# Kernel optimization log

Measured on AMD Instinct MI355X. Metric: run time of the kernel, lower is better.

The kernel has to match this reference:

```python
import jax, jax.numpy as jnp
import numpy as np
import math

D_MODEL = 1024
NUM_HEADS = 16
HEAD_DIM = D_MODEL // NUM_HEADS
BATCH = 2
SEQ = 2048
NEG_INF = -1000000.0  # matches torch code's -1e6 fill


def setup_inputs() -> dict:
    key = jax.random.key(0)
    ks = jax.random.split(key, 10)
    s = 1.0 / math.sqrt(D_MODEL)
    inp = {
        "X": jax.random.normal(ks[0], (BATCH, SEQ, D_MODEL), dtype=jnp.float32),
        "Wq": jax.random.uniform(ks[1], (D_MODEL, D_MODEL), minval=-s, maxval=s, dtype=jnp.float32),
        "bq": jnp.zeros((D_MODEL,), jnp.float32),
        "Wk": jax.random.uniform(ks[2], (D_MODEL, D_MODEL), minval=-s, maxval=s, dtype=jnp.float32),
        "bk": jnp.zeros((D_MODEL,), jnp.float32),
        "Wv": jax.random.uniform(ks[3], (D_MODEL, D_MODEL), minval=-s, maxval=s, dtype=jnp.float32),
        "bv": jnp.zeros((D_MODEL,), jnp.float32),
        "Wo": jax.random.uniform(ks[4], (D_MODEL, D_MODEL), minval=-s, maxval=s, dtype=jnp.float32),
        "bo": jnp.zeros((D_MODEL,), jnp.float32),
        "valid_lens": jax.random.randint(ks[5], (BATCH, NUM_HEADS), 1, SEQ + 1, dtype=jnp.int64)
        if jax.config.jax_enable_x64 else
        jax.random.randint(ks[5], (BATCH, NUM_HEADS), 1, SEQ + 1, dtype=jnp.int32),
    }
    return inp


def _split_heads(Y, B, S):
    # (B, S, D) -> (B*H, S, head_dim), matching transpose_qkv
    return Y.reshape(B, S, NUM_HEADS, HEAD_DIM).transpose(0, 2, 1, 3).reshape(B * NUM_HEADS, S, HEAD_DIM)


def reference(X, Wq, bq, Wk, bk, Wv, bv, Wo, bo, valid_lens):
    B, S, D = X.shape
    q = _split_heads(X @ Wq.T + bq, B, S)
    k = _split_heads(X @ Wk.T + bk, B, S)
    v = _split_heads(X @ Wv.T + bv, B, S)
    scores = jnp.einsum("bqd,bkd->bqk", q, k) / math.sqrt(HEAD_DIM)  # (B*H, S, S)
    # Faithful to torch code: 2-D valid_lens reshaped to (B*H,), mask over
    # the first two dims -> entire query rows j >= valid_len set to -1e6.
    row_mask = jnp.arange(S)[None, :] < valid_lens.reshape(-1)[:, None]  # (B*H, S)
    scores = jnp.where(row_mask[:, :, None], scores, NEG_INF)
    attn = jax.nn.softmax(scores, axis=-1)
    out = jnp.einsum("bqk,bkd->bqd", attn, v)  # (B*H, S, head_dim)
    out = out.reshape(B, NUM_HEADS, S, HEAD_DIM).transpose(0, 2, 1, 3).reshape(B, S, D)
    return out @ Wo.T + bo
```

## Files before the change

### kernel.cpp

```cpp
#include <hip/hip_runtime.h>

#define SQ 2048
#define DM 1024
#define NH 16
#define HD 64

typedef __bf16 bf16x8 __attribute__((ext_vector_type(8)));
typedef float f32x4 __attribute__((ext_vector_type(4)));
typedef unsigned short u16;
typedef unsigned int u32;

__device__ __forceinline__ u16 f2b(float f) {
  union { float f; u32 u; } c; c.f = f;
  return (u16)((c.u + 0x7FFFu + ((c.u >> 16) & 1u)) >> 16);
}

__device__ __forceinline__ void gll16(const void* g, void* l) {
  __builtin_amdgcn_global_load_lds(
      (const __attribute__((address_space(1))) void*)g,
      (__attribute__((address_space(3))) void*)l, 16, 0, 0);
}

__global__ void __launch_bounds__(256) conv_bf16(
    const float* __restrict__ X,
    const float* __restrict__ Wq, const float* __restrict__ Wk,
    const float* __restrict__ Wv, const float* __restrict__ Wo,
    u16* __restrict__ Xb, u16* __restrict__ Wqb, u16* __restrict__ Wkb,
    u16* __restrict__ Wvb, u16* __restrict__ Wob) {
  const size_t e = ((size_t)blockIdx.x * 256 + threadIdx.x) * 8;
  const float* src; u16* dst; size_t rel;
  if (e < 4194304u)      { src = X;  dst = Xb;  rel = e; }
  else if (e < 5242880u) { src = Wq; dst = Wqb; rel = e - 4194304u; }
  else if (e < 6291456u) { src = Wk; dst = Wkb; rel = e - 5242880u; }
  else if (e < 7340032u) { src = Wv; dst = Wvb; rel = e - 6291456u; }
  else                   { src = Wo; dst = Wob; rel = e - 7340032u; }
  float4 a = *(const float4*)(src + rel);
  float4 b = *(const float4*)(src + rel + 4);
  union { u16 h[8]; uint4 v; } o;
  o.h[0] = f2b(a.x); o.h[1] = f2b(a.y); o.h[2] = f2b(a.z); o.h[3] = f2b(a.w);
  o.h[4] = f2b(b.x); o.h[5] = f2b(b.y); o.h[6] = f2b(b.z); o.h[7] = f2b(b.w);
  *(uint4*)(dst + rel) = o.v;
}

__global__ void __launch_bounds__(256) mean_v2(
    const u16* __restrict__ Vt, const int* __restrict__ vlen,
    u16* __restrict__ Ao, int* __restrict__ wl) {
  __shared__ float part[256];
  __shared__ float smv[64];
  const int bh = blockIdx.x, c8 = blockIdx.y;
  const int t = threadIdx.x, d = t >> 2, c = t & 3;
  const u16* row = Vt + ((size_t)bh * HD + d) * SQ + c * 512;
  float s = 0.f;
  for (int i = 0; i < 64; ++i) {
    bf16x8 v = *(const bf16x8*)(row + i * 8);
    s += ((float)v[0] + (float)v[1]) + ((float)v[2] + (float)v[3])
       + ((float)v[4] + (float)v[5]) + ((float)v[6] + (float)v[7]);
  }
  part[t] = s;
  __syncthreads();
  if (c == 0) {
    const float tot = (part[t] + part[t + 1]) + (part[t + 2] + part[t + 3]);
    smv[d] = tot * (1.0f / 2048.0f);
  }
  __syncthreads();

  const int vl = vlen[bh];
  const int ft = (vl + 63) >> 6;
  const int b = bh >> 4, h = bh & 15;
  const int c16 = t & 15, r16 = t >> 4;
  union { u16 h4[4]; uint2 u; } pv;
#pragma unroll
  for (int j = 0; j < 4; ++j) pv.h4[j] = f2b(smv[c16 * 4 + j]);
  for (int ss = ft * 64 + c8 * 16 + r16; ss < SQ; ss += 128)
    *(uint2*)(Ao + ((size_t)(b * SQ + ss)) * DM + h * HD + c16 * 4) = pv.u;

  if (bh == 0 && c8 == 0) {
    __shared__ int nts[32], off[32];
    if (t < 32) {
      int nt = (vlen[t] + 63) >> 6;
      if (nt > 32) nt = 32;
      nts[t] = nt;
    }
    __syncthreads();
    if (t == 0) {
      int acc = 0;
      for (int i = 0; i < 32; ++i) { off[i] = acc; acc += nts[i]; }
      wl[0] = acc;
    }
    __syncthreads();
    if (t < 32) {
      const int o = off[t], nt = nts[t];
      for (int q = 0; q < nt; ++q) wl[1 + o + q] = (t << 5) | q;
    }
  }
}

__global__ void __launch_bounds__(256, 3) qkv_gemm(
    const u16* __restrict__ Xb, const u16* __restrict__ Wqkv,
    const float* __restrict__ bq, const float* __restrict__ bk, const float* __restrict__ bv,
    const int* __restrict__ vlen,
    u16* __restrict__ Qb, u16* __restrict__ Kb, u16* __restrict__ Vt) {
  __shared__ u16 sA[3][4096];
  __shared__ u16 sB[3][4096];
  const int id = blockIdx.x;
  const int swz = (id & 7) * 96 + (id >> 3);
  const int bx = swz % 24, by = swz / 24;
  const int m0 = by * 128, n0 = bx * 128;
  const int mode = n0 >> 10;
  const float* bias = (mode == 0) ? bq : (mode == 1) ? bk : bv;

  if (mode == 0) {
    const int bb = m0 >> 11, s0 = m0 & 2047, h0 = n0 >> 6;
    if (s0 >= vlen[bb * NH + h0] && s0 >= vlen[bb * NH + h0 + 1]) return;
  }

  const int t = threadIdx.x, l = t & 63, w = t >> 6;
  const int wr = w >> 1, wc = w & 1, lg = l >> 4, li = l & 15;

  int srcOff[2];
#pragma unroll
  for (int j = 0; j < 2; ++j) {
    const int g = w * 2 + j;
    const int row = g * 16 + (l >> 2);
    const int colsrc = ((l & 3) * 8) ^ (((row >> 3) & 1) << 4);
    srcOff[j] = row * DM + colsrc;
  }
  const u16* Abase = Xb + (size_t)m0 * DM;
  const u16* Bbase = Wqkv + (size_t)n0 * DM;

  auto stage = [&](int buf, int kt) {
#pragma unroll
    for (int j = 0; j < 2; ++j) {
      gll16(Abase + srcOff[j] + kt * 32, &sA[buf][(w * 2 + j) * 512]);
      gll16(Bbase + srcOff[j] + kt * 32, &sB[buf][(w * 2 + j) * 512]);
    }
  };

  f32x4 acc[4][4];
  f32x4 z4 = {0.f, 0.f, 0.f, 0.f};
#pragma unroll
  for (int i = 0; i < 4; ++i)
#pragma unroll
    for (int j = 0; j < 4; ++j) acc[i][j] = z4;

  stage(0, 0);
  stage(1, 1);
  for (int kt = 0; kt < 32; ++kt) {
    const int bsel = kt % 3;
    if (kt < 31) asm volatile("s_waitcnt vmcnt(4)" ::: "memory");
    else         asm volatile("s_waitcnt vmcnt(0)" ::: "memory");
    __builtin_amdgcn_s_barrier();
    asm volatile("" ::: "memory");

    bf16x8 aF[4], bF[4];
#pragma unroll
    for (int mi = 0; mi < 4; ++mi) {
      const int rl = wr * 64 + mi * 16 + li;
      aF[mi] = *(const bf16x8*)(&sA[bsel][rl * 32 + ((lg * 8) ^ (((rl >> 3) & 1) << 4))]);
    }
#pragma unroll
    for (int ni = 0; ni < 4; ++ni) {
      const int rn = wc * 64 + ni * 16 + li;
      bF[ni] = *(const bf16x8*)(&sB[bsel][rn * 32 + ((lg * 8) ^ (((rn >> 3) & 1) << 4))]);
    }
    if (kt + 2 < 32) stage((kt + 2) % 3, kt + 2);

    __builtin_amdgcn_s_setprio(1);
#pragma unroll
    for (int mi = 0; mi < 4; ++mi)
#pragma unroll
      for (int ni = 0; ni < 4; ++ni)
        acc[mi][ni] = __builtin_amdgcn_mfma_f32_16x16x32_bf16(aF[mi], bF[ni], acc[mi][ni], 0, 0, 0);
    __builtin_amdgcn_s_setprio(0);
  }

#pragma unroll
  for (int mi = 0; mi < 4; ++mi) {
    const int m = m0 + wr * 64 + mi * 16 + lg * 4;
    const int b = m >> 11;
    const int s = m & 2047;
#pragma unroll
    for (int ni = 0; ni < 4; ++ni) {
      const int n = n0 + wc * 64 + ni * 16 + li;
      const int nn = n - (mode << 10);
      const int h = nn >> 6, dd = nn & 63;
      const float bia = bias[nn];
      const size_t bh = (size_t)(b * NH + h);
      if (mode == 2) {
        union { u16 h4[4]; uint2 u; } pk;
#pragma unroll
        for (int r = 0; r < 4; ++r) pk.h4[r] = f2b(acc[mi][ni][r] + bia);
        *(uint2*)(Vt + (bh * HD + dd) * SQ + s) = pk.u;
      } else {
#pragma unroll
        for (int r = 0; r < 4; ++r) {
          const float val = acc[mi][ni][r] + bia;
          const int ss = s + r;
          if (mode == 0) Qb[(bh * SQ + ss) * HD + dd] = f2b(val * 0.180336880f);
          else           Kb[(bh * SQ + ss) * HD + dd] = f2b(val);
        }
      }
    }
  }
}

__global__ void __launch_bounds__(256) out_gemm(
    const u16* __restrict__ Ag, const u16* __restrict__ Wob,
    const float* __restrict__ bo, float* __restrict__ out) {
  __shared__ u16 sA[2][2048];
  __shared__ u16 sB[2][4096];
  const int t = threadIdx.x, l = t & 63, w = t >> 6;
  const int wr = w >> 1, wc = w & 1, lg = l >> 4, li = l & 15;
  const int m0 = blockIdx.y * 64, n0 = blockIdx.x * 128;

  auto stage = [&](int buf, int kt) {
    {
      const int s = w * 64 + l;
      const int r = s >> 2, cc = s & 3;
      gll16(Ag + (size_t)(m0 + r) * DM + kt * 32 + cc * 8, &sA[buf][w * 512]);
    }
#pragma unroll
    for (int c = 0; c < 2; ++c) {
      const int g = w * 2 + c;
      const int s = g * 64 + l;
      const int r = s >> 2, cc = s & 3;
      gll16(Wob + (size_t)(n0 + r) * DM + kt * 32 + cc * 8, &sB[buf][g * 512]);
    }
  };

  f32x4 acc[2][4];
  f32x4 z4 = {0.f, 0.f, 0.f, 0.f};
#pragma unroll
  for (int i = 0; i < 2; ++i)
#pragma unroll
    for (int j = 0; j < 4; ++j) acc[i][j] = z4;

  stage(0, 0);
  __syncthreads();
  int cur = 0;
  for (int kt = 0; kt < DM / 32; ++kt) {
    if (kt + 1 < DM / 32) stage(cur ^ 1, kt + 1);
    bf16x8 aF[2], bF[4];
#pragma unroll
    for (int mi = 0; mi < 2; ++mi)
      aF[mi] = *(const bf16x8*)(&sA[cur][(wr * 32 + mi * 16 + li) * 32 + lg * 8]);
#pragma unroll
    for (int ni = 0; ni < 4; ++ni)
      bF[ni] = *(const bf16x8*)(&sB[cur][(wc * 64 + ni * 16 + li) * 32 + lg * 8]);
#pragma unroll
    for (int mi = 0; mi < 2; ++mi)
#pragma unroll
      for (int ni = 0; ni < 4; ++ni)
        acc[mi][ni] = __builtin_amdgcn_mfma_f32_16x16x32_bf16(aF[mi], bF[ni], acc[mi][ni], 0, 0, 0);
    __syncthreads();
    cur ^= 1;
  }

#pragma unroll
  for (int mi = 0; mi < 2; ++mi) {
    const int m = m0 + wr * 32 + mi * 16 + lg * 4;
#pragma unroll
    for (int ni = 0; ni < 4; ++ni) {
      const int n = n0 + wc * 64 + ni * 16 + li;
      const float bia = bo[n];
#pragma unroll
      for (int r = 0; r < 4; ++r)
        out[(size_t)(m + r) * DM + n] = acc[mi][ni][r] + bia;
    }
  }
}

__global__ void __launch_bounds__(256, 2) attn_v15(
    const u16* __restrict__ Qb, const u16* __restrict__ Kb, const u16* __restrict__ Vt,
    const int* __restrict__ vlen, const int* __restrict__ wl, u16* __restrict__ Ao) {
  __shared__ u16 sKV[4][10240];
  const int t = threadIdx.x, w = t >> 6, l = t & 63, lg = l >> 4, li = l & 15;
  const int nit = wl[0];

  int kOff[4], vOff[4];
#pragma unroll
  for (int i = 0; i < 4; ++i) {
    {
      const int s = i * 64 + l, row = s >> 3, c = s & 7;
      const int csrc = c ^ (row & 7);
      const int sig = (((row >> 2) & 3) << 3) | (((row >> 4) & 1) << 2) | (row & 3);
      kOff[i] = sig * HD + csrc * 8;
    }
    {
      const int s = i * 64 + l, d = s >> 2, c = s & 3;
      const int csrc = c ^ ((d >> 2) & 3);
      vOff[i] = d * SQ + csrc * 8;
    }
  }

  u16* sw = &sKV[w][0];
  f32x4* op = (f32x4*)&sKV[0][0];
  float* lp = (float*)((char*)&sKV[0][0] + 65536);

  for (int it = blockIdx.x; it < nit; it += gridDim.x) {
    const int item = wl[1 + it];
    const int bh = item >> 5, qt = item & 31;
    const int vl = vlen[bh];
    const int q0 = qt * 64;
    const int b = bh >> 4, h = bh & 15;
    const u16* Qh = Qb + (size_t)bh * SQ * HD;
    const u16* Kh = Kb + (size_t)bh * SQ * HD;
    const u16* Vh = Vt + (size_t)bh * HD * SQ;
    const int k0 = w * 512;

    bf16x8 qf[4][2];
#pragma unroll
    for (int g = 0; g < 4; ++g) {
      const bool mq = (q0 + g * 16 + li) >= vl;
#pragma unroll
      for (int kk = 0; kk < 2; ++kk) {
        qf[g][kk] = *(const bf16x8*)(Qh + (size_t)(q0 + g * 16 + li) * HD + kk * 32 + lg * 8);
        if (mq) {
          union { u32 u[4]; bf16x8 v; } z; z.u[0] = z.u[1] = z.u[2] = z.u[3] = 0;
          qf[g][kk] = z.v;
        }
      }
    }

    auto stageK = [&](int buf, int tt) {
      const u16* kb = Kh + (size_t)(k0 + tt * 32) * HD;
#pragma unroll
      for (int i = 0; i < 4; ++i) gll16(kb + kOff[i], sw + buf * 2048 + i * 512);
    };
    auto stageV = [&](int buf, int tt) {
      const u16* vb = Vh + (size_t)(k0 + tt * 32);
#pragma unroll
      for (int i = 0; i < 4; ++i) gll16(vb + vOff[i], sw + 6144 + buf * 2048 + i * 512);
    };

    f32x4 z4 = {0.f, 0.f, 0.f, 0.f};
    f32x4 acc[4][4];
    float lr[4] = {0.f, 0.f, 0.f, 0.f};
#pragma unroll
    for (int g = 0; g < 4; ++g)
#pragma unroll
      for (int n2 = 0; n2 < 4; ++n2) acc[g][n2] = z4;

    stageV(0, 0); stageK(0, 0); stageK(1, 1);
    for (int tt = 0; tt < 16; ++tt) {
      if (tt + 1 < 16) stageV((tt + 1) & 1, tt + 1);
      if (tt + 2 < 16) stageK((tt + 2) % 3, tt + 2);
      if (tt <= 13)      asm volatile("s_waitcnt vmcnt(12)" ::: "memory");
      else if (tt == 14) asm volatile("s_waitcnt vmcnt(8)" ::: "memory");
      else               asm volatile("s_waitcnt vmcnt(0)" ::: "memory");
      const u16* kb_ = sw + (tt % 3) * 2048;
      const u16* vb_ = sw + 6144 + (tt & 1) * 2048;

      bf16x8 kf[2][2], vf[4];
#pragma unroll
      for (int ni = 0; ni < 2; ++ni) {
        const int row = ni * 16 + li;
        kf[ni][0] = *(const bf16x8*)(kb_ + row * 64 + ((lg ^ (row & 7)) * 8));
        kf[ni][1] = *(const bf16x8*)(kb_ + row * 64 + (((4 + lg) ^ (row & 7)) * 8));
      }
#pragma unroll
      for (int n2 = 0; n2 < 4; ++n2) {
        const int d = n2 * 16 + li;
        vf[n2] = *(const bf16x8*)(vb_ + d * 32 + ((lg ^ ((d >> 2) & 3)) * 8));
      }

      f32x4 s0a[4], s1a[4];
      __builtin_amdgcn_s_setprio(1);
#pragma unroll
      for (int g = 0; g < 4; ++g) {
        s0a[g] = __builtin_amdgcn_mfma_f32_16x16x32_bf16(kf[0][0], qf[g][0], z4, 0, 0, 0);
        s1a[g] = __builtin_amdgcn_mfma_f32_16x16x32_bf16(kf[1][0], qf[g][0], z4, 0, 0, 0);
      }
#pragma unroll
      for (int g = 0; g < 4; ++g) {
        s0a[g] = __builtin_amdgcn_mfma_f32_16x16x32_bf16(kf[0][1], qf[g][1], s0a[g], 0, 0, 0);
        s1a[g] = __builtin_amdgcn_mfma_f32_16x16x32_bf16(kf[1][1], qf[g][1], s1a[g], 0, 0, 0);
      }
      __builtin_amdgcn_s_setprio(0);

      bf16x8 Pv[4];
#pragma unroll
      for (int g = 0; g < 4; ++g) {
        union { __bf16 e[8]; bf16x8 v; } P;
        float ls = 0.f;
#pragma unroll
        for (int r = 0; r < 4; ++r) {
          const float p0 = __builtin_amdgcn_exp2f(s0a[g][r]);
          const float p1 = __builtin_amdgcn_exp2f(s1a[g][r]);
          P.e[r]     = (__bf16)p0;
          P.e[4 + r] = (__bf16)p1;
          ls += p0 + p1;
        }
        lr[g] += ls;
        Pv[g] = P.v;
      }

      __builtin_amdgcn_s_setprio(1);
#pragma unroll
      for (int g = 0; g < 4; ++g)
#pragma unroll
        for (int n2 = 0; n2 < 4; ++n2)
          acc[g][n2] = __builtin_amdgcn_mfma_f32_16x16x32_bf16(vf[n2], Pv[g], acc[g][n2], 0, 0, 0);
      __builtin_amdgcn_s_setprio(0);
    }

    __syncthreads();
#pragma unroll
    for (int g = 0; g < 4; ++g) {
#pragma unroll
      for (int n2 = 0; n2 < 4; ++n2)
        op[(((w * 4) + g) * 4 + n2) * 64 + l] = acc[g][n2];
      float v = lr[g];
      v += __shfl_xor(v, 16);
      v += __shfl_xor(v, 32);
      if (lg == 0) lp[(w * 4 + g) * 16 + li] = v;
    }
    __syncthreads();

    const int g = w;
    const float lf = lp[(0 * 4 + g) * 16 + li] + lp[(1 * 4 + g) * 16 + li]
                   + lp[(2 * 4 + g) * 16 + li] + lp[(3 * 4 + g) * 16 + li];
    const float inv = 1.0f / lf;
    const size_t rowb = ((size_t)(b * SQ + q0 + g * 16 + li)) * DM + h * HD;
#pragma unroll
    for (int n2 = 0; n2 < 4; ++n2) {
      f32x4 s = op[((0 * 4 + g) * 4 + n2) * 64 + l];
      s += op[((1 * 4 + g) * 4 + n2) * 64 + l];
      s += op[((2 * 4 + g) * 4 + n2) * 64 + l];
      s += op[((3 * 4 + g) * 4 + n2) * 64 + l];
      union { __bf16 h2[4]; uint2 u; } ov;
#pragma unroll
      for (int r = 0; r < 4; ++r) ov.h2[r] = (__bf16)(s[r] * inv);
      *(uint2*)(Ao + rowb + n2 * 16 + lg * 4) = ov.u;
    }
    __syncthreads();
  }
}

extern "C" void kernel_launch(void* const* d_in, const int* in_sizes, int n_in,
                              void* d_out, int out_size, void* d_ws, size_t ws_size,
                              hipStream_t stream) {
  const float* X  = (const float*)d_in[0];
  const float* Wq = (const float*)d_in[1];
  const float* bq = (const float*)d_in[2];
  const float* Wk = (const float*)d_in[3];
  const float* bk = (const float*)d_in[4];
  const float* Wv = (const float*)d_in[5];
  const float* bv = (const float*)d_in[6];
  const float* Wo = (const float*)d_in[7];
  const float* bo = (const float*)d_in[8];
  const int* vlen = (const int*)d_in[9];

  char* ws = (char*)d_ws;
  u16* Qb  = (u16*)(ws);
  u16* Kb  = (u16*)(ws + (size_t)8388608);
  u16* Vt  = (u16*)(ws + (size_t)16777216);
  u16* Xb  = (u16*)(ws + (size_t)25165824);
  u16* Ao  = Xb;
  u16* Wqb = (u16*)(ws + (size_t)33554432);
  u16* Wkb = (u16*)(ws + (size_t)35651584);
  u16* Wvb = (u16*)(ws + (size_t)37748736);
  u16* Wob = (u16*)(ws + (size_t)39845888);

  int* wl = (int*)((char*)d_out + 8192);

  dim3 blk(256);
  conv_bf16<<<4096, blk, 0, stream>>>(X, Wq, Wk, Wv, Wo, Xb, Wqb, Wkb, Wvb, Wob);
  qkv_gemm<<<768, blk, 0, stream>>>(Xb, Wqb, bq, bk, bv, vlen, Qb, Kb, Vt);
  mean_v2<<<dim3(32, 8), blk, 0, stream>>>(Vt, vlen, Ao, wl);
  attn_v15<<<512, blk, 0, stream>>>(Qb, Kb, Vt, vlen, wl, Ao);
  out_gemm<<<dim3(8, 64), blk, 0, stream>>>(Ao, Wob, bo, (float*)d_out);
}
```

Baseline: 116.6 us.

## Fuse masked-row mean fill and work-list build into attention kernel

Removes the separate mean_v2 kernel by having each attention block compute its own work assignment from valid_lens in shared memory. Blocks past the active count compute the V column mean and write it to fully masked query rows, and active blocks run one attention tile each. The launch grows to 1024 blocks with no persistent loop. This saves a kernel launch and the global work-list round trip. In exchange, each masked-tile block recomputes the V mean for its head redundantly.

```diff
diff --git a/kernel.cpp b/kernel.cpp
--- a/kernel.cpp
+++ b/kernel.cpp
@@ -42,59 +42,6 @@
   *(uint4*)(dst + rel) = o.v;
 }
 
-__global__ void __launch_bounds__(256) mean_v2(
-    const u16* __restrict__ Vt, const int* __restrict__ vlen,
-    u16* __restrict__ Ao, int* __restrict__ wl) {
-  __shared__ float part[256];
-  __shared__ float smv[64];
-  const int bh = blockIdx.x, c8 = blockIdx.y;
-  const int t = threadIdx.x, d = t >> 2, c = t & 3;
-  const u16* row = Vt + ((size_t)bh * HD + d) * SQ + c * 512;
-  float s = 0.f;
-  for (int i = 0; i < 64; ++i) {
-    bf16x8 v = *(const bf16x8*)(row + i * 8);
-    s += ((float)v[0] + (float)v[1]) + ((float)v[2] + (float)v[3])
-       + ((float)v[4] + (float)v[5]) + ((float)v[6] + (float)v[7]);
-  }
-  part[t] = s;
-  __syncthreads();
-  if (c == 0) {
-    const float tot = (part[t] + part[t + 1]) + (part[t + 2] + part[t + 3]);
-    smv[d] = tot * (1.0f / 2048.0f);
-  }
-  __syncthreads();
-
-  const int vl = vlen[bh];
-  const int ft = (vl + 63) >> 6;
-  const int b = bh >> 4, h = bh & 15;
-  const int c16 = t & 15, r16 = t >> 4;
-  union { u16 h4[4]; uint2 u; } pv;
-#pragma unroll
-  for (int j = 0; j < 4; ++j) pv.h4[j] = f2b(smv[c16 * 4 + j]);
-  for (int ss = ft * 64 + c8 * 16 + r16; ss < SQ; ss += 128)
-    *(uint2*)(Ao + ((size_t)(b * SQ + ss)) * DM + h * HD + c16 * 4) = pv.u;
-
-  if (bh == 0 && c8 == 0) {
-    __shared__ int nts[32], off[32];
-    if (t < 32) {
-      int nt = (vlen[t] + 63) >> 6;
-      if (nt > 32) nt = 32;
-      nts[t] = nt;
-    }
-    __syncthreads();
-    if (t == 0) {
-      int acc = 0;
-      for (int i = 0; i < 32; ++i) { off[i] = acc; acc += nts[i]; }
-      wl[0] = acc;
-    }
-    __syncthreads();
-    if (t < 32) {
-      const int o = off[t], nt = nts[t];
-      for (int q = 0; q < nt; ++q) wl[1 + o + q] = (t << 5) | q;
-    }
-  }
-}
-
 __global__ void __launch_bounds__(256, 3) qkv_gemm(
     const u16* __restrict__ Xb, const u16* __restrict__ Wqkv,
     const float* __restrict__ bq, const float* __restrict__ bk, const float* __restrict__ bv,
@@ -270,12 +217,78 @@
   }
 }
 
-__global__ void __launch_bounds__(256, 2) attn_v15(
+__global__ void __launch_bounds__(256, 2) attn_v17(
     const u16* __restrict__ Qb, const u16* __restrict__ Kb, const u16* __restrict__ Vt,
-    const int* __restrict__ vlen, const int* __restrict__ wl, u16* __restrict__ Ao) {
+    const int* __restrict__ vlen, u16* __restrict__ Ao) {
   __shared__ u16 sKV[4][10240];
+  __shared__ int s_nt[32], s_off[32], s_nact;
   const int t = threadIdx.x, w = t >> 6, l = t & 63, lg = l >> 4, li = l & 15;
-  const int nit = wl[0];
+
+  if (t < 32) {
+    int nt = (vlen[t] + 63) >> 6;
+    if (nt > 32) nt = 32;
+    s_nt[t] = nt;
+  }
+  __syncthreads();
+  if (t == 0) {
+    int acc = 0;
+    for (int i = 0; i < 32; ++i) { s_off[i] = acc; acc += s_nt[i]; }
+    s_nact = acc;
+  }
+  __syncthreads();
+
+  const int id = blockIdx.x;
+  const int nact = s_nact;
+  int bh, qt;
+  if (id < nact) {
+    int b = 0;
+    for (int i = 1; i < 32; ++i) if (s_off[i] <= id) b = i;
+    bh = b; qt = id - s_off[b];
+  } else {
+    const int j = id - nact;
+    int b = 0;
+    for (int i = 1; i < 32; ++i) if (32 * i - s_off[i] <= j) b = i;
+    bh = b; qt = s_nt[b] + (j - (32 * b - s_off[b]));
+  }
+  const int vl = vlen[bh];
+  const int q0 = qt * 64;
+  const int b_ = bh >> 4, h = bh & 15;
+  const u16* Vh = Vt + (size_t)bh * HD * SQ;
+
+  if (id >= nact) {
+    float* part = (float*)&sKV[0][0];
+    float* smv  = part + 256;
+    const int d = t >> 2, c = t & 3;
+    const u16* row = Vh + (size_t)d * SQ + c * 512;
+    float s = 0.f;
+    for (int i = 0; i < 64; ++i) {
+      bf16x8 v = *(const bf16x8*)(row + i * 8);
+      s += ((float)v[0] + (float)v[1]) + ((float)v[2] + (float)v[3])
+         + ((float)v[4] + (float)v[5]) + ((float)v[6] + (float)v[7]);
+    }
+    part[t] = s;
+    __syncthreads();
+    if (c == 0) {
+      const float tot = (part[t] + part[t + 1]) + (part[t + 2] + part[t + 3]);
+      smv[d] = tot * (1.0f / 2048.0f);
+    }
+    __syncthreads();
+    const int rrow = t >> 2;
+    const size_t rowb = ((size_t)(b_ * SQ + q0 + rrow)) * DM + h * HD;
+#pragma unroll
+    for (int k = 0; k < 4; ++k) {
+      const int gidx = (t & 3) + k * 4;
+      union { u16 h4[4]; uint2 u; } pv;
+#pragma unroll
+      for (int j = 0; j < 4; ++j) pv.h4[j] = f2b(smv[gidx * 4 + j]);
+      *(uint2*)(Ao + rowb + gidx * 4) = pv.u;
+    }
+    return;
+  }
+
+  const u16* Qh = Qb + (size_t)bh * SQ * HD;
+  const u16* Kh = Kb + (size_t)bh * SQ * HD;
+  const int k0 = w * 512;
 
   int kOff[4], vOff[4];
 #pragma unroll
@@ -297,143 +310,130 @@
   f32x4* op = (f32x4*)&sKV[0][0];
   float* lp = (float*)((char*)&sKV[0][0] + 65536);
 
-  for (int it = blockIdx.x; it < nit; it += gridDim.x) {
-    const int item = wl[1 + it];
-    const int bh = item >> 5, qt = item & 31;
-    const int vl = vlen[bh];
-    const int q0 = qt * 64;
-    const int b = bh >> 4, h = bh & 15;
-    const u16* Qh = Qb + (size_t)bh * SQ * HD;
-    const u16* Kh = Kb + (size_t)bh * SQ * HD;
-    const u16* Vh = Vt + (size_t)bh * HD * SQ;
-    const int k0 = w * 512;
-
-    bf16x8 qf[4][2];
+  bf16x8 qf[4][2];
+#pragma unroll
+  for (int g = 0; g < 4; ++g) {
+    const bool mq = (q0 + g * 16 + li) >= vl;
+#pragma unroll
+    for (int kk = 0; kk < 2; ++kk) {
+      qf[g][kk] = *(const bf16x8*)(Qh + (size_t)(q0 + g * 16 + li) * HD + kk * 32 + lg * 8);
+      if (mq) {
+        union { u32 u[4]; bf16x8 v; } z; z.u[0] = z.u[1] = z.u[2] = z.u[3] = 0;
+        qf[g][kk] = z.v;
+      }
+    }
+  }
+
+  auto stageK = [&](int buf, int tt) {
+    const u16* kb = Kh + (size_t)(k0 + tt * 32) * HD;
+#pragma unroll
+    for (int i = 0; i < 4; ++i) gll16(kb + kOff[i], sw + buf * 2048 + i * 512);
+  };
+  auto stageV = [&](int buf, int tt) {
+    const u16* vb = Vh + (size_t)(k0 + tt * 32);
+#pragma unroll
+    for (int i = 0; i < 4; ++i) gll16(vb + vOff[i], sw + 6144 + buf * 2048 + i * 512);
+  };
+
+  f32x4 z4 = {0.f, 0.f, 0.f, 0.f};
+  f32x4 acc[4][4];
+  float lr[4] = {0.f, 0.f, 0.f, 0.f};
+#pragma unroll
+  for (int g = 0; g < 4; ++g)
+#pragma unroll
+    for (int n2 = 0; n2 < 4; ++n2) acc[g][n2] = z4;
+
+  stageV(0, 0); stageK(0, 0); stageK(1, 1);
+  for (int tt = 0; tt < 16; ++tt) {
+    if (tt + 1 < 16) stageV((tt + 1) & 1, tt + 1);
+    if (tt + 2 < 16) stageK((tt + 2) % 3, tt + 2);
+    if (tt <= 13)      asm volatile("s_waitcnt vmcnt(12)" ::: "memory");
+    else if (tt == 14) asm volatile("s_waitcnt vmcnt(8)" ::: "memory");
+    else               asm volatile("s_waitcnt vmcnt(0)" ::: "memory");
+    const u16* kb_ = sw + (tt % 3) * 2048;
+    const u16* vb_ = sw + 6144 + (tt & 1) * 2048;
+
+    bf16x8 kf[2][2], vf[4];
+#pragma unroll
+    for (int ni = 0; ni < 2; ++ni) {
+      const int row = ni * 16 + li;
+      kf[ni][0] = *(const bf16x8*)(kb_ + row * 64 + ((lg ^ (row & 7)) * 8));
+      kf[ni][1] = *(const bf16x8*)(kb_ + row * 64 + (((4 + lg) ^ (row & 7)) * 8));
+    }
+#pragma unroll
+    for (int n2 = 0; n2 < 4; ++n2) {
+      const int d = n2 * 16 + li;
+      vf[n2] = *(const bf16x8*)(vb_ + d * 32 + ((lg ^ ((d >> 2) & 3)) * 8));
+    }
+
+    f32x4 s0a[4], s1a[4];
+    __builtin_amdgcn_s_setprio(1);
 #pragma unroll
     for (int g = 0; g < 4; ++g) {
-      const bool mq = (q0 + g * 16 + li) >= vl;
-#pragma unroll
-      for (int kk = 0; kk < 2; ++kk) {
-        qf[g][kk] = *(const bf16x8*)(Qh + (size_t)(q0 + g * 16 + li) * HD + kk * 32 + lg * 8);
-        if (mq) {
-          union { u32 u[4]; bf16x8 v; } z; z.u[0] = z.u[1] = z.u[2] = z.u[3] = 0;
-          qf[g][kk] = z.v;
-        }
+      s0a[g] = __builtin_amdgcn_mfma_f32_16x16x32_bf16(kf[0][0], qf[g][0], z4, 0, 0, 0);
+      s1a[g] = __builtin_amdgcn_mfma_f32_16x16x32_bf16(kf[1][0], qf[g][0], z4, 0, 0, 0);
+    }
+#pragma unroll
+    for (int g = 0; g < 4; ++g) {
+      s0a[g] = __builtin_amdgcn_mfma_f32_16x16x32_bf16(kf[0][1], qf[g][1], s0a[g], 0, 0, 0);
+      s1a[g] = __builtin_amdgcn_mfma_f32_16x16x32_bf16(kf[1][1], qf[g][1], s1a[g], 0, 0, 0);
+    }
+    __builtin_amdgcn_s_setprio(0);
+
+    bf16x8 Pv[4];
+#pragma unroll
+    for (int g = 0; g < 4; ++g) {
+      union { __bf16 e[8]; bf16x8 v; } P;
+      float ls = 0.f;
+#pragma unroll
+      for (int r = 0; r < 4; ++r) {
+        const float p0 = __builtin_amdgcn_exp2f(s0a[g][r]);
+        const float p1 = __builtin_amdgcn_exp2f(s1a[g][r]);
+        P.e[r]     = (__bf16)p0;
+        P.e[4 + r] = (__bf16)p1;
+        ls += p0 + p1;
       }
-    }
-
-    auto stageK = [&](int buf, int tt) {
-      const u16* kb = Kh + (size_t)(k0 + tt * 32) * HD;
-#pragma unroll
-      for (int i = 0; i < 4; ++i) gll16(kb + kOff[i], sw + buf * 2048 + i * 512);
-    };
-    auto stageV = [&](int buf, int tt) {
-      const u16* vb = Vh + (size_t)(k0 + tt * 32);
-#pragma unroll
-      for (int i = 0; i < 4; ++i) gll16(vb + vOff[i], sw + 6144 + buf * 2048 + i * 512);
-    };
-
-    f32x4 z4 = {0.f, 0.f, 0.f, 0.f};
-    f32x4 acc[4][4];
-    float lr[4] = {0.f, 0.f, 0.f, 0.f};
+      lr[g] += ls;
+      Pv[g] = P.v;
+    }
+
+    __builtin_amdgcn_s_setprio(1);
 #pragma unroll
     for (int g = 0; g < 4; ++g)
 #pragma unroll
-      for (int n2 = 0; n2 < 4; ++n2) acc[g][n2] = z4;
-
-    stageV(0, 0); stageK(0, 0); stageK(1, 1);
-    for (int tt = 0; tt < 16; ++tt) {
-      if (tt + 1 < 16) stageV((tt + 1) & 1, tt + 1);
-      if (tt + 2 < 16) stageK((tt + 2) % 3, tt + 2);
-      if (tt <= 13)      asm volatile("s_waitcnt vmcnt(12)" ::: "memory");
-      else if (tt == 14) asm volatile("s_waitcnt vmcnt(8)" ::: "memory");
-      else               asm volatile("s_waitcnt vmcnt(0)" ::: "memory");
-      const u16* kb_ = sw + (tt % 3) * 2048;
-      const u16* vb_ = sw + 6144 + (tt & 1) * 2048;
-
-      bf16x8 kf[2][2], vf[4];
-#pragma unroll
-      for (int ni = 0; ni < 2; ++ni) {
-        const int row = ni * 16 + li;
-        kf[ni][0] = *(const bf16x8*)(kb_ + row * 64 + ((lg ^ (row & 7)) * 8));
-        kf[ni][1] = *(const bf16x8*)(kb_ + row * 64 + (((4 + lg) ^ (row & 7)) * 8));
-      }
-#pragma unroll
-      for (int n2 = 0; n2 < 4; ++n2) {
-        const int d = n2 * 16 + li;
-        vf[n2] = *(const bf16x8*)(vb_ + d * 32 + ((lg ^ ((d >> 2) & 3)) * 8));
-      }
-
-      f32x4 s0a[4], s1a[4];
-      __builtin_amdgcn_s_setprio(1);
-#pragma unroll
-      for (int g = 0; g < 4; ++g) {
-        s0a[g] = __builtin_amdgcn_mfma_f32_16x16x32_bf16(kf[0][0], qf[g][0], z4, 0, 0, 0);
-        s1a[g] = __builtin_amdgcn_mfma_f32_16x16x32_bf16(kf[1][0], qf[g][0], z4, 0, 0, 0);
-      }
-#pragma unroll
-      for (int g = 0; g < 4; ++g) {
-        s0a[g] = __builtin_amdgcn_mfma_f32_16x16x32_bf16(kf[0][1], qf[g][1], s0a[g], 0, 0, 0);
-        s1a[g] = __builtin_amdgcn_mfma_f32_16x16x32_bf16(kf[1][1], qf[g][1], s1a[g], 0, 0, 0);
-      }
-      __builtin_amdgcn_s_setprio(0);
-
-      bf16x8 Pv[4];
-#pragma unroll
-      for (int g = 0; g < 4; ++g) {
-        union { __bf16 e[8]; bf16x8 v; } P;
-        float ls = 0.f;
-#pragma unroll
-        for (int r = 0; r < 4; ++r) {
-          const float p0 = __builtin_amdgcn_exp2f(s0a[g][r]);
-          const float p1 = __builtin_amdgcn_exp2f(s1a[g][r]);
-          P.e[r]     = (__bf16)p0;
-          P.e[4 + r] = (__bf16)p1;
-          ls += p0 + p1;
-        }
-        lr[g] += ls;
-        Pv[g] = P.v;
-      }
-
-      __builtin_amdgcn_s_setprio(1);
-#pragma unroll
-      for (int g = 0; g < 4; ++g)
-#pragma unroll
-        for (int n2 = 0; n2 < 4; ++n2)
-          acc[g][n2] = __builtin_amdgcn_mfma_f32_16x16x32_bf16(vf[n2], Pv[g], acc[g][n2], 0, 0, 0);
-      __builtin_amdgcn_s_setprio(0);
-    }
-
-    __syncthreads();
-#pragma unroll
-    for (int g = 0; g < 4; ++g) {
-#pragma unroll
       for (int n2 = 0; n2 < 4; ++n2)
-        op[(((w * 4) + g) * 4 + n2) * 64 + l] = acc[g][n2];
-      float v = lr[g];
-      v += __shfl_xor(v, 16);
-      v += __shfl_xor(v, 32);
-      if (lg == 0) lp[(w * 4 + g) * 16 + li] = v;
-    }
-    __syncthreads();
-
-    const int g = w;
-    const float lf = lp[(0 * 4 + g) * 16 + li] + lp[(1 * 4 + g) * 16 + li]
-                   + lp[(2 * 4 + g) * 16 + li] + lp[(3 * 4 + g) * 16 + li];
-    const float inv = 1.0f / lf;
-    const size_t rowb = ((size_t)(b * SQ + q0 + g * 16 + li)) * DM + h * HD;
-#pragma unroll
-    for (int n2 = 0; n2 < 4; ++n2) {
-      f32x4 s = op[((0 * 4 + g) * 4 + n2) * 64 + l];
-      s += op[((1 * 4 + g) * 4 + n2) * 64 + l];
-      s += op[((2 * 4 + g) * 4 + n2) * 64 + l];
-      s += op[((3 * 4 + g) * 4 + n2) * 64 + l];
-      union { __bf16 h2[4]; uint2 u; } ov;
-#pragma unroll
-      for (int r = 0; r < 4; ++r) ov.h2[r] = (__bf16)(s[r] * inv);
-      *(uint2*)(Ao + rowb + n2 * 16 + lg * 4) = ov.u;
-    }
-    __syncthreads();
+        acc[g][n2] = __builtin_amdgcn_mfma_f32_16x16x32_bf16(vf[n2], Pv[g], acc[g][n2], 0, 0, 0);
+    __builtin_amdgcn_s_setprio(0);
+  }
+
+  __syncthreads();
+#pragma unroll
+  for (int g = 0; g < 4; ++g) {
+#pragma unroll
+    for (int n2 = 0; n2 < 4; ++n2)
+      op[(((w * 4) + g) * 4 + n2) * 64 + l] = acc[g][n2];
+    float v = lr[g];
+    v += __shfl_xor(v, 16);
+    v += __shfl_xor(v, 32);
+    if (lg == 0) lp[(w * 4 + g) * 16 + li] = v;
+  }
+  __syncthreads();
+
+  const int g = w;
+  const float lf = lp[(0 * 4 + g) * 16 + li] + lp[(1 * 4 + g) * 16 + li]
+                 + lp[(2 * 4 + g) * 16 + li] + lp[(3 * 4 + g) * 16 + li];
+  const float inv = 1.0f / lf;
+  const size_t rowb = ((size_t)(b_ * SQ + q0 + g * 16 + li)) * DM + h * HD;
+#pragma unroll
+  for (int n2 = 0; n2 < 4; ++n2) {
+    f32x4 s = op[((0 * 4 + g) * 4 + n2) * 64 + l];
+    s += op[((1 * 4 + g) * 4 + n2) * 64 + l];
+    s += op[((2 * 4 + g) * 4 + n2) * 64 + l];
+    s += op[((3 * 4 + g) * 4 + n2) * 64 + l];
+    union { __bf16 h2[4]; uint2 u; } ov;
+#pragma unroll
+    for (int r = 0; r < 4; ++r) ov.h2[r] = (__bf16)(s[r] * inv);
+    *(uint2*)(Ao + rowb + n2 * 16 + lg * 4) = ov.u;
   }
 }
 
@@ -462,12 +462,9 @@
   u16* Wvb = (u16*)(ws + (size_t)37748736);
   u16* Wob = (u16*)(ws + (size_t)39845888);
 
-  int* wl = (int*)((char*)d_out + 8192);
-
   dim3 blk(256);
   conv_bf16<<<4096, blk, 0, stream>>>(X, Wq, Wk, Wv, Wo, Xb, Wqb, Wkb, Wvb, Wob);
   qkv_gemm<<<768, blk, 0, stream>>>(Xb, Wqb, bq, bk, bv, vlen, Qb, Kb, Vt);
-  mean_v2<<<dim3(32, 8), blk, 0, stream>>>(Vt, vlen, Ao, wl);
-  attn_v15<<<512, blk, 0, stream>>>(Qb, Kb, Vt, vlen, wl, Ao);
+  attn_v17<<<1024, blk, 0, stream>>>(Qb, Kb, Vt, vlen, Ao);
   out_gemm<<<dim3(8, 64), blk, 0, stream>>>(Ao, Wob, bo, (float*)d_out);
 }
```

Result: slower. 142.7 us (+22.5%).

## Shrink QKV GEMM tile to 64x128 with double buffering and more blocks

Applied to the files above, without the earlier changes.

Replaces the 128x128 triple-buffered QKV projection GEMM with a 64x128 tile, double-buffered LDS and a plain syncthreads pipeline, and launches twice as many blocks. The aim is finer-grained work so early-exit skipping of masked Q rows wastes less and the 256 CUs are better load balanced. In exchange it drops the XOR swizzle on LDS (possible bank conflicts), the setprio hints and the deeper prefetch. It also lowers operand reuse per block, so more global and LDS traffic per FLOP.

```diff
diff --git a/kernel.cpp b/kernel.cpp
--- a/kernel.cpp
+++ b/kernel.cpp
@@ -95,17 +95,19 @@
   }
 }
 
-__global__ void __launch_bounds__(256, 3) qkv_gemm(
+__global__ void __launch_bounds__(256) qkv_gemm64(
     const u16* __restrict__ Xb, const u16* __restrict__ Wqkv,
     const float* __restrict__ bq, const float* __restrict__ bk, const float* __restrict__ bv,
     const int* __restrict__ vlen,
     u16* __restrict__ Qb, u16* __restrict__ Kb, u16* __restrict__ Vt) {
-  __shared__ u16 sA[3][4096];
-  __shared__ u16 sB[3][4096];
+  __shared__ u16 sA[2][2048];
+  __shared__ u16 sB[2][4096];
+  const int t = threadIdx.x, l = t & 63, w = t >> 6;
+  const int wr = w >> 1, wc = w & 1, lg = l >> 4, li = l & 15;
   const int id = blockIdx.x;
-  const int swz = (id & 7) * 96 + (id >> 3);
+  const int swz = (id & 7) * 192 + (id >> 3);
   const int bx = swz % 24, by = swz / 24;
-  const int m0 = by * 128, n0 = bx * 128;
+  const int m0 = by * 64, n0 = bx * 128;
   const int mode = n0 >> 10;
   const float* bias = (mode == 0) ? bq : (mode == 1) ? bk : bv;
 
@@ -114,69 +116,52 @@
     if (s0 >= vlen[bb * NH + h0] && s0 >= vlen[bb * NH + h0 + 1]) return;
   }
 
-  const int t = threadIdx.x, l = t & 63, w = t >> 6;
-  const int wr = w >> 1, wc = w & 1, lg = l >> 4, li = l & 15;
-
-  int srcOff[2];
-#pragma unroll
-  for (int j = 0; j < 2; ++j) {
-    const int g = w * 2 + j;
-    const int row = g * 16 + (l >> 2);
-    const int colsrc = ((l & 3) * 8) ^ (((row >> 3) & 1) << 4);
-    srcOff[j] = row * DM + colsrc;
-  }
-  const u16* Abase = Xb + (size_t)m0 * DM;
-  const u16* Bbase = Wqkv + (size_t)n0 * DM;
-
   auto stage = [&](int buf, int kt) {
-#pragma unroll
-    for (int j = 0; j < 2; ++j) {
-      gll16(Abase + srcOff[j] + kt * 32, &sA[buf][(w * 2 + j) * 512]);
-      gll16(Bbase + srcOff[j] + kt * 32, &sB[buf][(w * 2 + j) * 512]);
+    {
+      const int s = w * 64 + l;
+      const int r = s >> 2, cc = s & 3;
+      gll16(Xb + (size_t)(m0 + r) * DM + kt * 32 + cc * 8, &sA[buf][w * 512]);
+    }
+#pragma unroll
+    for (int c = 0; c < 2; ++c) {
+      const int g = w * 2 + c;
+      const int s = g * 64 + l;
+      const int r = s >> 2, cc = s & 3;
+      gll16(Wqkv + (size_t)(n0 + r) * DM + kt * 32 + cc * 8, &sB[buf][g * 512]);
     }
   };
 
-  f32x4 acc[4][4];
+  f32x4 acc[2][4];
   f32x4 z4 = {0.f, 0.f, 0.f, 0.f};
 #pragma unroll
-  for (int i = 0; i < 4; ++i)
+  for (int i = 0; i < 2; ++i)
 #pragma unroll
     for (int j = 0; j < 4; ++j) acc[i][j] = z4;
 
   stage(0, 0);
-  stage(1, 1);
-  for (int kt = 0; kt < 32; ++kt) {
-    const int bsel = kt % 3;
-    if (kt < 31) asm volatile("s_waitcnt vmcnt(4)" ::: "memory");
-    else         asm volatile("s_waitcnt vmcnt(0)" ::: "memory");
-    __builtin_amdgcn_s_barrier();
-    asm volatile("" ::: "memory");
-
-    bf16x8 aF[4], bF[4];
-#pragma unroll
-    for (int mi = 0; mi < 4; ++mi) {
-      const int rl = wr * 64 + mi * 16 + li;
-      aF[mi] = *(const bf16x8*)(&sA[bsel][rl * 32 + ((lg * 8) ^ (((rl >> 3) & 1) << 4))]);
-    }
-#pragma unroll
-    for (int ni = 0; ni < 4; ++ni) {
-      const int rn = wc * 64 + ni * 16 + li;
-      bF[ni] = *(const bf16x8*)(&sB[bsel][rn * 32 + ((lg * 8) ^ (((rn >> 3) & 1) << 4))]);
-    }
-    if (kt + 2 < 32) stage((kt + 2) % 3, kt + 2);
-
-    __builtin_amdgcn_s_setprio(1);
-#pragma unroll
-    for (int mi = 0; mi < 4; ++mi)
+  __syncthreads();
+  int cur = 0;
+  for (int kt = 0; kt < DM / 32; ++kt) {
+    if (kt + 1 < DM / 32) stage(cur ^ 1, kt + 1);
+    bf16x8 aF[2], bF[4];
+#pragma unroll
+    for (int mi = 0; mi < 2; ++mi)
+      aF[mi] = *(const bf16x8*)(&sA[cur][(wr * 32 + mi * 16 + li) * 32 + lg * 8]);
+#pragma unroll
+    for (int ni = 0; ni < 4; ++ni)
+      bF[ni] = *(const bf16x8*)(&sB[cur][(wc * 64 + ni * 16 + li) * 32 + lg * 8]);
+#pragma unroll
+    for (int mi = 0; mi < 2; ++mi)
 #pragma unroll
       for (int ni = 0; ni < 4; ++ni)
         acc[mi][ni] = __builtin_amdgcn_mfma_f32_16x16x32_bf16(aF[mi], bF[ni], acc[mi][ni], 0, 0, 0);
-    __builtin_amdgcn_s_setprio(0);
-  }
-
-#pragma unroll
-  for (int mi = 0; mi < 4; ++mi) {
-    const int m = m0 + wr * 64 + mi * 16 + lg * 4;
+    __syncthreads();
+    cur ^= 1;
+  }
+
+#pragma unroll
+  for (int mi = 0; mi < 2; ++mi) {
+    const int m = m0 + wr * 32 + mi * 16 + lg * 4;
     const int b = m >> 11;
     const int s = m & 2047;
 #pragma unroll
@@ -466,7 +451,7 @@
 
   dim3 blk(256);
   conv_bf16<<<4096, blk, 0, stream>>>(X, Wq, Wk, Wv, Wo, Xb, Wqb, Wkb, Wvb, Wob);
-  qkv_gemm<<<768, blk, 0, stream>>>(Xb, Wqb, bq, bk, bv, vlen, Qb, Kb, Vt);
+  qkv_gemm64<<<1536, blk, 0, stream>>>(Xb, Wqb, bq, bk, bv, vlen, Qb, Kb, Vt);
   mean_v2<<<dim3(32, 8), blk, 0, stream>>>(Vt, vlen, Ao, wl);
   attn_v15<<<512, blk, 0, stream>>>(Qb, Kb, Vt, vlen, wl, Ao);
   out_gemm<<<dim3(8, 64), blk, 0, stream>>>(Ao, Wob, bo, (float*)d_out);
```

New measurement: 140.2 us. +20.3%, slower.
